# Performance work log

Hardware: AMD Instinct MI355X
Metric: run time of the kernel (lower is better)

## Reference

```python
import jax, jax.numpy as jnp
import numpy as np

TEMPERATURE = 0.5
BATCH_SIZE = 4096
EPS = 1e-8  # torch.nn.CosineSimilarity default eps


def setup_inputs() -> dict:
    key = jax.random.key(0)
    k1, k2 = jax.random.split(key)
    z1 = jax.random.normal(k1, (BATCH_SIZE, 256), dtype=jnp.float32)
    z2 = jax.random.normal(k2, (BATCH_SIZE, 256), dtype=jnp.float32)
    return {"z1": z1, "z2": z2}


def reference(z1, z2):
    B = z1.shape[0]
    N = 2 * B
    reps = jnp.concatenate([z1, z2], axis=0)  # [N, D]
    # Cosine similarity (torch clamps each norm to eps before dividing)
    norms = jnp.maximum(jnp.linalg.norm(reps, axis=1, keepdims=True), EPS)
    z = reps / norms
    sim = z @ z.T  # [N, N] cosine similarity matrix

    # positives: diagonals at offsets +B and -B (they are identical by symmetry,
    # but keep the original concat order: [diag(+B), diag(-B)])
    l_pos = jnp.diagonal(sim, offset=B)
    r_pos = jnp.diagonal(sim, offset=-B)
    positives = jnp.concatenate([l_pos, r_pos])  # [N]

    inv_t = 1.0 / TEMPERATURE
    pos_logit = positives * inv_t  # logits[:, 0]

    # negatives are all off-diagonal entries of each row (the positive pair is
    # thus present twice in the logits, faithful to the original). CE with
    # label 0 => loss_i = logsumexp(logits_i) - logits_i[0].
    neg_logits = jnp.where(jnp.eye(N, dtype=bool), -jnp.inf, sim * inv_t)
    lse = jnp.logaddexp(pos_logit, jax.scipy.special.logsumexp(neg_logits, axis=1))
    loss = jnp.sum(lse - pos_logit) / N
    return loss
```

## Files before the change

kernel.cpp:

```cpp
#include <hip/hip_runtime.h>
#include <hip/hip_bf16.h>
#include <cstdint>
#include <cstddef>
#include <math.h>

#define BSZ   4096
#define NROW  8192
#define DIM   256
#define INV_T 2.0f
#define EPS_N 1e-8f

typedef __attribute__((ext_vector_type(8))) short bf16x8;
typedef __attribute__((ext_vector_type(4))) float f32x4;

__device__ __forceinline__ unsigned short f2bf(float x) {
    __hip_bfloat16 h = __float2bfloat16(x);
    return __builtin_bit_cast(unsigned short, h);
}

__device__ __forceinline__ void load_lds16(const void* g, void* l) {
    __builtin_amdgcn_global_load_lds(
        (const __attribute__((address_space(1))) void*)g,
        (__attribute__((address_space(3))) void*)l,
        16, 0, 0);
}

__global__ __launch_bounds__(256)
void nt_normalize(const float* __restrict__ z1,
                  const float* __restrict__ z2,
                  __hip_bfloat16* __restrict__ zn,
                  float* __restrict__ rowsum) {
    const int wave = threadIdx.x >> 6;
    const int lane = threadIdx.x & 63;
    const int row  = blockIdx.x * 4 + wave;
    const float* src = (row < BSZ) ? (z1 + (size_t)row * DIM)
                                   : (z2 + (size_t)(row - BSZ) * DIM);
    const float4 v = ((const float4*)src)[lane];
    float ss = v.x * v.x + v.y * v.y + v.z * v.z + v.w * v.w;
    #pragma unroll
    for (int off = 32; off; off >>= 1) ss += __shfl_xor(ss, off);
    const float rinv = 1.0f / fmaxf(sqrtf(ss), EPS_N);
    ushort4 o;
    o.x = f2bf(v.x * rinv);
    o.y = f2bf(v.y * rinv);
    o.z = f2bf(v.z * rinv);
    o.w = f2bf(v.w * rinv);
    ((ushort4*)(zn + (size_t)row * DIM))[lane] = o;
    if (lane == 0) rowsum[row] = 0.0f;
}

__global__ __launch_bounds__(256)
void nt_gram(const __hip_bfloat16* __restrict__ zn,
             float* __restrict__ rowsum,
             float* __restrict__ pos) {
    const int l = blockIdx.x;
    int bi = (int)((129.0 - sqrt(16641.0 - 8.0 * (double)l)) * 0.5);
    while (64 * (bi + 1) - (bi + 1) * bi / 2 <= l) ++bi;
    while (64 * bi - bi * (bi - 1) / 2 > l) --bi;
    const int bj = bi + (l - (64 * bi - bi * (bi - 1) / 2));

    __shared__ __hip_bfloat16 As[128 * 64];
    __shared__ __hip_bfloat16 Bs[128 * 64];

    const int t    = threadIdx.x;
    const int lane = t & 63;
    const int wave = t >> 6;
    const int wrow = (wave >> 1) * 64;
    const int wcol = (wave & 1) * 64;

    f32x4 acc[4][4] = {};

    const __hip_bfloat16* Ag = zn + (size_t)bi * 128 * DIM;
    const __hip_bfloat16* Bg = zn + (size_t)bj * 128 * DIM;

    const int srow = t >> 3;
    const int sc   = (t & 7) ^ (srow & 7);

    const int q   = lane >> 4;
    const int r16 = lane & 15;
    const int sw  = r16 & 7;

    for (int k0 = 0; k0 < DIM; k0 += 64) {
        #pragma unroll
        for (int p = 0; p < 4; ++p) {
            const int row = p * 32 + srow;
            load_lds16(Ag + (size_t)row * DIM + k0 + sc * 8,
                       (char*)As + p * 4096 + t * 16);
            load_lds16(Bg + (size_t)row * DIM + k0 + sc * 8,
                       (char*)Bs + p * 4096 + t * 16);
        }
        __syncthreads();

        #pragma unroll
        for (int kk = 0; kk < 64; kk += 32) {
            const int cc = (kk >> 3) + q;
            const int cpos = (cc ^ sw) << 4;
            bf16x8 af[4], bfr[4];
            #pragma unroll
            for (int mi = 0; mi < 4; ++mi) {
                const int m = wrow + mi * 16 + r16;
                af[mi] = *(const bf16x8*)((const char*)As + m * 128 + cpos);
            }
            #pragma unroll
            for (int ni = 0; ni < 4; ++ni) {
                const int n = wcol + ni * 16 + r16;
                bfr[ni] = *(const bf16x8*)((const char*)Bs + n * 128 + cpos);
            }
            #pragma unroll
            for (int mi = 0; mi < 4; ++mi)
                #pragma unroll
                for (int ni = 0; ni < 4; ++ni)
                    acc[mi][ni] = __builtin_amdgcn_mfma_f32_16x16x32_bf16(
                        af[mi], bfr[ni], acc[mi][ni], 0, 0, 0);
        }
        __syncthreads();
    }

    const int c = lane & 15;
    const bool diag_block = (bi == bj);
    float colp[4] = {0.f, 0.f, 0.f, 0.f};

    #pragma unroll
    for (int mi = 0; mi < 4; ++mi) {
        #pragma unroll
        for (int r = 0; r < 4; ++r) {
            const int grow = bi * 128 + wrow + mi * 16 + q * 4 + r;
            float s = 0.f;
            #pragma unroll
            for (int ni = 0; ni < 4; ++ni) {
                const int gcol = bj * 128 + wcol + ni * 16 + c;
                const float val = acc[mi][ni][r];
                float e = __expf(val * INV_T);
                e = (grow == gcol) ? 0.f : e;
                s += e;
                colp[ni] += e;
                if (gcol == grow + BSZ) {
                    pos[grow] = val;
                    pos[gcol] = val;
                }
            }
            s += __shfl_xor(s, 1);
            s += __shfl_xor(s, 2);
            s += __shfl_xor(s, 4);
            s += __shfl_xor(s, 8);
            if (c == 0) atomicAdd(&rowsum[grow], s);
        }
    }
    if (!diag_block) {
        #pragma unroll
        for (int ni = 0; ni < 4; ++ni) {
            float cs = colp[ni];
            cs += __shfl_xor(cs, 16);
            cs += __shfl_xor(cs, 32);
            if (q == 0) atomicAdd(&rowsum[bj * 128 + wcol + ni * 16 + c], cs);
        }
    }
}

__global__ __launch_bounds__(1024)
void nt_finalize(const float* __restrict__ rowsum,
                 const float* __restrict__ pos,
                 float* __restrict__ out) {
    float v = 0.f;
    for (int i = threadIdx.x; i < NROW; i += 1024) {
        const float pl = pos[i] * INV_T;
        v += logf(__expf(pl) + rowsum[i]) - pl;
    }
    #pragma unroll
    for (int off = 32; off; off >>= 1) v += __shfl_xor(v, off);
    __shared__ float red[16];
    if ((threadIdx.x & 63) == 0) red[threadIdx.x >> 6] = v;
    __syncthreads();
    if (threadIdx.x == 0) {
        float s = 0.f;
        #pragma unroll
        for (int w = 0; w < 16; ++w) s += red[w];
        out[0] = s * (1.0f / NROW);
    }
}

extern "C" void kernel_launch(void* const* d_in, const int* in_sizes, int n_in,
                              void* d_out, int out_size, void* d_ws, size_t ws_size,
                              hipStream_t stream) {
    const float* z1 = (const float*)d_in[0];
    const float* z2 = (const float*)d_in[1];
    float* out = (float*)d_out;

    __hip_bfloat16* zn = (__hip_bfloat16*)d_ws;
    float* rowsum = (float*)((char*)d_ws + (size_t)NROW * DIM * 2);
    float* pos    = rowsum + NROW;

    nt_normalize<<<NROW / 4, 256, 0, stream>>>(z1, z2, zn, rowsum);
    nt_gram<<<2080, 256, 0, stream>>>(zn, rowsum, pos);
    nt_finalize<<<1, 1024, 0, stream>>>(rowsum, pos, out);
}
```

Baseline: 105.1 us.

## Load MFMA fragments directly from global and move diagonal masking out of the epilogue

The LDS staging of the A/B tiles is removed. Each wave now loads its bf16x8 fragments straight from global memory into registers, double-buffered across the 8 k-steps, which drops both __syncthreads barriers. The diagonal mask is gone from the epilogue: the bf16 self-dot of each row is computed in the normalize kernel and its exponential is subtracted in the finalize step. Positive-pair extraction is limited to the blocks and waves that hold that diagonal, and exp uses exp2f with a folded constant. This cuts LDS traffic and per-element compare work, at the cost of redundant global/L2 reads with no LDS reuse across waves, and a subtraction whose accuracy depends on the MFMA self-dot matching the recomputed sum.

```diff
diff --git a/kernel.cpp b/kernel.cpp
--- a/kernel.cpp
+++ b/kernel.cpp
@@ -9,6 +9,7 @@
 #define DIM   256
 #define INV_T 2.0f
 #define EPS_N 1e-8f
+#define CE    2.8853900817779268f
 
 typedef __attribute__((ext_vector_type(8))) short bf16x8;
 typedef __attribute__((ext_vector_type(4))) float f32x4;
@@ -17,19 +18,17 @@
     __hip_bfloat16 h = __float2bfloat16(x);
     return __builtin_bit_cast(unsigned short, h);
 }
-
-__device__ __forceinline__ void load_lds16(const void* g, void* l) {
-    __builtin_amdgcn_global_load_lds(
-        (const __attribute__((address_space(1))) void*)g,
-        (__attribute__((address_space(3))) void*)l,
-        16, 0, 0);
+__device__ __forceinline__ float bf2f(unsigned short u) {
+    __hip_bfloat16 h = __builtin_bit_cast(__hip_bfloat16, u);
+    return __bfloat162float(h);
 }
 
 __global__ __launch_bounds__(256)
 void nt_normalize(const float* __restrict__ z1,
                   const float* __restrict__ z2,
                   __hip_bfloat16* __restrict__ zn,
-                  float* __restrict__ rowsum) {
+                  float* __restrict__ rowsum,
+                  float* __restrict__ sii) {
     const int wave = threadIdx.x >> 6;
     const int lane = threadIdx.x & 63;
     const int row  = blockIdx.x * 4 + wave;
@@ -46,7 +45,11 @@
     o.z = f2bf(v.z * rinv);
     o.w = f2bf(v.w * rinv);
     ((ushort4*)(zn + (size_t)row * DIM))[lane] = o;
-    if (lane == 0) rowsum[row] = 0.0f;
+    float bx = bf2f(o.x), by = bf2f(o.y), bz = bf2f(o.z), bw = bf2f(o.w);
+    float s2 = bx * bx + by * by + bz * bz + bw * bw;
+    #pragma unroll
+    for (int off = 32; off; off >>= 1) s2 += __shfl_xor(s2, off);
+    if (lane == 0) { sii[row] = s2; rowsum[row] = 0.0f; }
 }
 
 __global__ __launch_bounds__(256)
@@ -59,94 +62,69 @@
     while (64 * bi - bi * (bi - 1) / 2 > l) --bi;
     const int bj = bi + (l - (64 * bi - bi * (bi - 1) / 2));
 
-    __shared__ __hip_bfloat16 As[128 * 64];
-    __shared__ __hip_bfloat16 Bs[128 * 64];
-
-    const int t    = threadIdx.x;
-    const int lane = t & 63;
-    const int wave = t >> 6;
+    const int lane = threadIdx.x & 63;
+    const int wave = threadIdx.x >> 6;
     const int wrow = (wave >> 1) * 64;
     const int wcol = (wave & 1) * 64;
+    const int q    = lane >> 4;
+    const int r16  = lane & 15;
+
+    const __hip_bfloat16* Arow = zn + (size_t)(bi * 128 + wrow + r16) * DIM + q * 8;
+    const __hip_bfloat16* Brow = zn + (size_t)(bj * 128 + wcol + r16) * DIM + q * 8;
 
     f32x4 acc[4][4] = {};
+    bf16x8 a[2][4], b[2][4];
 
-    const __hip_bfloat16* Ag = zn + (size_t)bi * 128 * DIM;
-    const __hip_bfloat16* Bg = zn + (size_t)bj * 128 * DIM;
-
-    const int srow = t >> 3;
-    const int sc   = (t & 7) ^ (srow & 7);
-
-    const int q   = lane >> 4;
-    const int r16 = lane & 15;
-    const int sw  = r16 & 7;
-
-    for (int k0 = 0; k0 < DIM; k0 += 64) {
-        #pragma unroll
-        for (int p = 0; p < 4; ++p) {
-            const int row = p * 32 + srow;
-            load_lds16(Ag + (size_t)row * DIM + k0 + sc * 8,
-                       (char*)As + p * 4096 + t * 16);
-            load_lds16(Bg + (size_t)row * DIM + k0 + sc * 8,
-                       (char*)Bs + p * 4096 + t * 16);
-        }
-        __syncthreads();
-
-        #pragma unroll
-        for (int kk = 0; kk < 64; kk += 32) {
-            const int cc = (kk >> 3) + q;
-            const int cpos = (cc ^ sw) << 4;
-            bf16x8 af[4], bfr[4];
+    #pragma unroll
+    for (int mi = 0; mi < 4; ++mi) {
+        a[0][mi] = *(const bf16x8*)(Arow + (size_t)mi * 16 * DIM);
+        b[0][mi] = *(const bf16x8*)(Brow + (size_t)mi * 16 * DIM);
+    }
+    #pragma unroll
+    for (int ks = 0; ks < 8; ++ks) {
+        const int cur = ks & 1, nxt = cur ^ 1;
+        if (ks < 7) {
+            const __hip_bfloat16* An = Arow + (ks + 1) * 32;
+            const __hip_bfloat16* Bn = Brow + (ks + 1) * 32;
             #pragma unroll
             for (int mi = 0; mi < 4; ++mi) {
-                const int m = wrow + mi * 16 + r16;
-                af[mi] = *(const bf16x8*)((const char*)As + m * 128 + cpos);
+                a[nxt][mi] = *(const bf16x8*)(An + (size_t)mi * 16 * DIM);
+                b[nxt][mi] = *(const bf16x8*)(Bn + (size_t)mi * 16 * DIM);
             }
+        }
+        #pragma unroll
+        for (int mi = 0; mi < 4; ++mi)
             #pragma unroll
-            for (int ni = 0; ni < 4; ++ni) {
-                const int n = wcol + ni * 16 + r16;
-                bfr[ni] = *(const bf16x8*)((const char*)Bs + n * 128 + cpos);
-            }
-            #pragma unroll
-            for (int mi = 0; mi < 4; ++mi)
-                #pragma unroll
-                for (int ni = 0; ni < 4; ++ni)
-                    acc[mi][ni] = __builtin_amdgcn_mfma_f32_16x16x32_bf16(
-                        af[mi], bfr[ni], acc[mi][ni], 0, 0, 0);
-        }
-        __syncthreads();
+            for (int ni = 0; ni < 4; ++ni)
+                acc[mi][ni] = __builtin_amdgcn_mfma_f32_16x16x32_bf16(
+                    a[cur][mi], b[cur][ni], acc[mi][ni], 0, 0, 0);
     }
 
     const int c = lane & 15;
-    const bool diag_block = (bi == bj);
     float colp[4] = {0.f, 0.f, 0.f, 0.f};
 
     #pragma unroll
     for (int mi = 0; mi < 4; ++mi) {
         #pragma unroll
         for (int r = 0; r < 4; ++r) {
-            const int grow = bi * 128 + wrow + mi * 16 + q * 4 + r;
             float s = 0.f;
             #pragma unroll
             for (int ni = 0; ni < 4; ++ni) {
-                const int gcol = bj * 128 + wcol + ni * 16 + c;
-                const float val = acc[mi][ni][r];
-                float e = __expf(val * INV_T);
-                e = (grow == gcol) ? 0.f : e;
+                const float e = exp2f(acc[mi][ni][r] * CE);
                 s += e;
                 colp[ni] += e;
-                if (gcol == grow + BSZ) {
-                    pos[grow] = val;
-                    pos[gcol] = val;
-                }
             }
             s += __shfl_xor(s, 1);
             s += __shfl_xor(s, 2);
             s += __shfl_xor(s, 4);
             s += __shfl_xor(s, 8);
-            if (c == 0) atomicAdd(&rowsum[grow], s);
+            if (c == 0) {
+                const int grow = bi * 128 + wrow + mi * 16 + q * 4 + r;
+                atomicAdd(&rowsum[grow], s);
+            }
         }
     }
-    if (!diag_block) {
+    if (bi != bj) {
         #pragma unroll
         for (int ni = 0; ni < 4; ++ni) {
             float cs = colp[ni];
@@ -155,16 +133,30 @@
             if (q == 0) atomicAdd(&rowsum[bj * 128 + wcol + ni * 16 + c], cs);
         }
     }
+    if (bj == bi + 32 && wrow == wcol) {
+        #pragma unroll
+        for (int mi = 0; mi < 4; ++mi)
+            #pragma unroll
+            for (int r = 0; r < 4; ++r)
+                if (c == q * 4 + r) {
+                    const int grow = bi * 128 + wrow + mi * 16 + q * 4 + r;
+                    const float val = acc[mi][mi][r];
+                    pos[grow] = val;
+                    pos[grow + BSZ] = val;
+                }
+    }
 }
 
 __global__ __launch_bounds__(1024)
 void nt_finalize(const float* __restrict__ rowsum,
                  const float* __restrict__ pos,
+                 const float* __restrict__ sii,
                  float* __restrict__ out) {
     float v = 0.f;
     for (int i = threadIdx.x; i < NROW; i += 1024) {
-        const float pl = pos[i] * INV_T;
-        v += logf(__expf(pl) + rowsum[i]) - pl;
+        const float pl  = pos[i] * INV_T;
+        const float neg = rowsum[i] - exp2f(sii[i] * CE);
+        v += logf(__expf(pl) + neg) - pl;
     }
     #pragma unroll
     for (int off = 32; off; off >>= 1) v += __shfl_xor(v, off);
@@ -189,8 +181,9 @@
     __hip_bfloat16* zn = (__hip_bfloat16*)d_ws;
     float* rowsum = (float*)((char*)d_ws + (size_t)NROW * DIM * 2);
     float* pos    = rowsum + NROW;
+    float* sii    = pos + NROW;
 
-    nt_normalize<<<NROW / 4, 256, 0, stream>>>(z1, z2, zn, rowsum);
+    nt_normalize<<<NROW / 4, 256, 0, stream>>>(z1, z2, zn, rowsum, sii);
     nt_gram<<<2080, 256, 0, stream>>>(zn, rowsum, pos);
-    nt_finalize<<<1, 1024, 0, stream>>>(rowsum, pos, out);
+    nt_finalize<<<1, 1024, 0, stream>>>(rowsum, pos, sii, out);
 }
```

Measured after the change: 157.6 us. +49.9%, slower.
